# Kernel tuning notes

Measured on AMD Instinct MI355X. Metric: run time of the kernel, lower is better.

The kernel has to match this reference:

```python
import jax, jax.numpy as jnp
import numpy as np

N_NODES = 50000
N_EDGES = 800000
EMB = 96
HID = 2 * EMB


def setup_inputs() -> dict:
    key = jax.random.key(0)
    ks = jax.random.split(key, 8)
    h = jax.random.normal(ks[0], (N_NODES, EMB), dtype=jnp.float32)
    edge_attr = jax.random.normal(ks[1], (N_EDGES, EMB), dtype=jnp.float32)
    src = jax.random.randint(ks[2], (N_EDGES,), 0, N_NODES, dtype=jnp.int32)
    dst = jax.random.randint(ks[3], (N_EDGES,), 0, N_NODES, dtype=jnp.int32)
    W1 = jax.random.normal(ks[4], (EMB, HID), dtype=jnp.float32) * (1.0 / np.sqrt(EMB))
    b1 = jnp.zeros((HID,), dtype=jnp.float32)
    W2 = jax.random.normal(ks[5], (HID, EMB), dtype=jnp.float32) * (1.0 / np.sqrt(HID))
    b2 = jnp.zeros((EMB,), dtype=jnp.float32)
    eps = jnp.zeros((1,), dtype=jnp.float32)
    return {"h": h, "edge_attr": edge_attr, "src": src, "dst": dst,
            "W1": W1, "b1": b1, "W2": W2, "b2": b2, "eps": eps}


def reference(h, edge_attr, src, dst, W1, b1, W2, b2, eps):
    # message: m_e = h[src_e] + edge_attr_e   -> [E, EMB]
    m = h[src] + edge_attr
    # reduce: sum messages per destination node -> [N, EMB]
    aggr = jax.ops.segment_sum(m, dst, num_segments=N_NODES)
    # 2-layer MLP: Linear(EMB, 2*EMB) -> ReLU -> Linear(2*EMB, EMB)
    hidden = jax.nn.relu(aggr @ W1 + b1)
    mlp_out = hidden @ W2 + b2
    # GIN update: (1 + eps) * h + MLP(aggr)
    out = (1.0 + eps[0]) * h + mlp_out
    return out
```

## Files before the change

### kernel.cpp

```cpp
#include <hip/hip_runtime.h>

#define N_NODES 50000
#define N_EDGES 800000
#define EMB 96
#define HID 192

typedef __attribute__((ext_vector_type(8))) short short8;
typedef __attribute__((ext_vector_type(4))) float f32x4;
typedef __attribute__((ext_vector_type(4))) unsigned short ushort4v;

static __device__ __forceinline__ unsigned short f2bf(float f) {
    union { float f; unsigned int u; } v; v.f = f;
    unsigned int u = v.u;
    return (unsigned short)((u + 0x7FFFu + ((u >> 16) & 1u)) >> 16);
}

__global__ __launch_bounds__(256) void hist_kernel(
    const int* __restrict__ dst, int* __restrict__ counts)
{
    int e = blockIdx.x * 256 + threadIdx.x;
    if (e < N_EDGES) atomicAdd(&counts[dst[e]], 1);
}

__global__ __launch_bounds__(1024) void scan_kernel(
    const int* __restrict__ counts, int* __restrict__ offsets)
{
    __shared__ int wave_sums[16];
    int t = threadIdx.x;
    int lane = t & 63, wave = t >> 6;
    int running = 0;
    for (int base = 0; base < N_NODES; base += 1024) {
        int v = (base + t < N_NODES) ? counts[base + t] : 0;
        int x = v;
        #pragma unroll
        for (int d = 1; d < 64; d <<= 1) {
            int y = __shfl_up(x, d);
            if (lane >= d) x += y;
        }
        if (lane == 63) wave_sums[wave] = x;
        __syncthreads();
        if (t < 16) {
            int s = wave_sums[t];
            #pragma unroll
            for (int d = 1; d < 16; d <<= 1) {
                int y = __shfl_up(s, d);
                if (t >= d) s += y;
            }
            wave_sums[t] = s;
        }
        __syncthreads();
        int woff = wave ? wave_sums[wave - 1] : 0;
        if (base + t < N_NODES) offsets[base + t] = running + woff + x - v;
        int total = wave_sums[15];
        __syncthreads();
        running += total;
    }
    if (t == 0) offsets[N_NODES] = running;
}

__global__ __launch_bounds__(256) void fill_kernel(
    const int* __restrict__ src, const int* __restrict__ dst,
    const int* __restrict__ offsets, int* __restrict__ cursor,
    int2* __restrict__ pairs)
{
    int e = blockIdx.x * 256 + threadIdx.x;
    if (e < N_EDGES) {
        int d = dst[e];
        int pos = offsets[d] + atomicAdd(&cursor[d], 1);
        pairs[pos] = make_int2(e, src[e]);
    }
}

__global__ __launch_bounds__(256) void conv_kernel(
    const float* __restrict__ W1, const float* __restrict__ W2,
    unsigned short* __restrict__ W1t, unsigned short* __restrict__ W2t)
{
    int i = blockIdx.x * 256 + threadIdx.x;
    if (i < EMB * HID) {
        int n = i / EMB, k = i % EMB;
        W1t[i] = f2bf(W1[(size_t)k * HID + n]);
    } else if (i < 2 * EMB * HID) {
        int j = i - EMB * HID;
        int n = j / HID, k = j % HID;
        W2t[j] = f2bf(W2[(size_t)k * EMB + n]);
    }
}

__global__ __launch_bounds__(192) void gather_kernel(
    const float4* __restrict__ h4, const float4* __restrict__ ea4,
    const int* __restrict__ offsets, const int2* __restrict__ pairs,
    unsigned short* __restrict__ aggr_bf)
{
    int n = blockIdx.x * 8 + threadIdx.x / 24;
    int c = threadIdx.x % 24;
    if (n >= N_NODES) return;
    int beg = offsets[n], end = offsets[n + 1];
    float4 acc = make_float4(0.f, 0.f, 0.f, 0.f);
    int i = beg;
    int2 p = (i < end) ? pairs[i] : make_int2(0, 0);
    while (i < end) {
        int2 cur = p;
        ++i;
        if (i < end) p = pairs[i];
        float4 a = ea4[(size_t)cur.x * 24 + c];
        float4 b = h4[(size_t)cur.y * 24 + c];
        acc.x += a.x + b.x;
        acc.y += a.y + b.y;
        acc.z += a.z + b.z;
        acc.w += a.w + b.w;
    }
    ushort4v o;
    o.x = f2bf(acc.x); o.y = f2bf(acc.y); o.z = f2bf(acc.z); o.w = f2bf(acc.w);
    *(ushort4v*)(aggr_bf + (size_t)n * EMB + c * 4) = o;
}

__global__ __launch_bounds__(256) void mlp1_mfma(
    const unsigned short* __restrict__ aggr_bf,
    const unsigned short* __restrict__ W1t,
    const float* __restrict__ b1,
    unsigned short* __restrict__ hidden_bf)
{
    __shared__ unsigned short sW[HID * 104];
    int t = threadIdx.x;
    const unsigned int* srcp = (const unsigned int*)W1t;
    for (int i = t; i < HID * (EMB / 2); i += 256) {
        int n = i / (EMB / 2), c = i % (EMB / 2);
        *(unsigned int*)&sW[n * 104 + c * 2] = srcp[(size_t)n * (EMB / 2) + c];
    }
    __syncthreads();
    int wave = t >> 6, lane = t & 63;
    int m0 = (blockIdx.x * 4 + wave) * 16;
    if (m0 >= N_NODES) return;
    int quad = lane >> 4, col = lane & 15;
    f32x4 acc[12];
    #pragma unroll
    for (int c = 0; c < 12; ++c) acc[c] = (f32x4){0.f, 0.f, 0.f, 0.f};
    int m = m0 + col;
    #pragma unroll
    for (int ks = 0; ks < 3; ++ks) {
        short8 af = *(const short8*)(aggr_bf + (size_t)m * EMB + ks * 32 + quad * 8);
        #pragma unroll
        for (int c = 0; c < 12; ++c) {
            short8 bf = *(const short8*)(sW + (c * 16 + col) * 104 + ks * 32 + quad * 8);
            acc[c] = __builtin_amdgcn_mfma_f32_16x16x32_bf16(af, bf, acc[c], 0, 0, 0);
        }
    }
    #pragma unroll
    for (int c = 0; c < 12; ++c) {
        float bias = b1[c * 16 + col];
        #pragma unroll
        for (int r = 0; r < 4; ++r) {
            int row = m0 + quad * 4 + r;
            float v = fmaxf(acc[c][r] + bias, 0.f);
            hidden_bf[(size_t)row * HID + c * 16 + col] = f2bf(v);
        }
    }
}

__global__ __launch_bounds__(256) void mlp2_mfma(
    const unsigned short* __restrict__ hidden_bf,
    const unsigned short* __restrict__ W2t,
    const float* __restrict__ b2,
    const float* __restrict__ h,
    const float* __restrict__ eps,
    float* __restrict__ out)
{
    __shared__ unsigned short sW[EMB * 200];
    int t = threadIdx.x;
    const unsigned int* srcp = (const unsigned int*)W2t;
    for (int i = t; i < EMB * (HID / 2); i += 256) {
        int n = i / (HID / 2), c = i % (HID / 2);
        *(unsigned int*)&sW[n * 200 + c * 2] = srcp[(size_t)n * (HID / 2) + c];
    }
    __syncthreads();
    int wave = t >> 6, lane = t & 63;
    int m0 = (blockIdx.x * 4 + wave) * 16;
    if (m0 >= N_NODES) return;
    int quad = lane >> 4, col = lane & 15;
    f32x4 acc[6];
    #pragma unroll
    for (int c = 0; c < 6; ++c) acc[c] = (f32x4){0.f, 0.f, 0.f, 0.f};
    int m = m0 + col;
    #pragma unroll
    for (int ks = 0; ks < 6; ++ks) {
        short8 af = *(const short8*)(hidden_bf + (size_t)m * HID + ks * 32 + quad * 8);
        #pragma unroll
        for (int c = 0; c < 6; ++c) {
            short8 bf = *(const short8*)(sW + (c * 16 + col) * 200 + ks * 32 + quad * 8);
            acc[c] = __builtin_amdgcn_mfma_f32_16x16x32_bf16(af, bf, acc[c], 0, 0, 0);
        }
    }
    float s = 1.f + eps[0];
    #pragma unroll
    for (int c = 0; c < 6; ++c) {
        float bias = b2[c * 16 + col];
        #pragma unroll
        for (int r = 0; r < 4; ++r) {
            int row = m0 + quad * 4 + r;
            size_t idx = (size_t)row * EMB + c * 16 + col;
            out[idx] = acc[c][r] + bias + s * h[idx];
        }
    }
}

extern "C" void kernel_launch(void* const* d_in, const int* in_sizes, int n_in,
                              void* d_out, int out_size, void* d_ws, size_t ws_size,
                              hipStream_t stream) {
    const float* h         = (const float*)d_in[0];
    const float* edge_attr = (const float*)d_in[1];
    const int*   src       = (const int*)d_in[2];
    const int*   dst       = (const int*)d_in[3];
    const float* W1        = (const float*)d_in[4];
    const float* b1        = (const float*)d_in[5];
    const float* W2        = (const float*)d_in[6];
    const float* b2        = (const float*)d_in[7];
    const float* eps       = (const float*)d_in[8];
    float* out = (float*)d_out;

    unsigned char* wsp = (unsigned char*)d_ws;
    unsigned short* aggr_bf   = (unsigned short*)wsp; wsp += (size_t)N_NODES * EMB * 2;
    unsigned short* hidden_bf = (unsigned short*)wsp; wsp += (size_t)N_NODES * HID * 2;
    unsigned short* W1t       = (unsigned short*)wsp; wsp += (size_t)EMB * HID * 2;
    unsigned short* W2t       = (unsigned short*)wsp; wsp += (size_t)EMB * HID * 2;
    int2* pairs   = (int2*)wsp; wsp += (size_t)N_EDGES * sizeof(int2);
    int*  offsets = (int*)wsp;  wsp += (size_t)(N_NODES + 1) * sizeof(int);
    int*  counts  = (int*)wsp;  wsp += (size_t)N_NODES * sizeof(int);
    int*  cursor  = (int*)wsp;

    hipMemsetAsync(counts, 0, (size_t)2 * N_NODES * sizeof(int), stream);

    hist_kernel<<<(N_EDGES + 255) / 256, 256, 0, stream>>>(dst, counts);
    scan_kernel<<<1, 1024, 0, stream>>>(counts, offsets);
    fill_kernel<<<(N_EDGES + 255) / 256, 256, 0, stream>>>(src, dst, offsets, cursor, pairs);
    conv_kernel<<<(2 * EMB * HID + 255) / 256, 256, 0, stream>>>(W1, W2, W1t, W2t);
    gather_kernel<<<(N_NODES + 7) / 8, 192, 0, stream>>>(
        (const float4*)h, (const float4*)edge_attr, offsets, pairs, aggr_bf);

    mlp1_mfma<<<(N_NODES / 16 + 3) / 4, 256, 0, stream>>>(aggr_bf, W1t, b1, hidden_bf);
    mlp2_mfma<<<(N_NODES / 16 + 3) / 4, 256, 0, stream>>>(hidden_bf, W2t, b2, h, eps, out);
}
```

Baseline: 613.1 us.

## Fuse MLP layers, merge hist/conv kernels, unroll gather, prefetch scan loads

```diff
diff --git a/kernel.cpp b/kernel.cpp
--- a/kernel.cpp
+++ b/kernel.cpp
@@ -5,6 +5,9 @@
 #define EMB 96
 #define HID 192
 
+#define HIST_BLOCKS ((N_EDGES + 255) / 256)
+#define CONV_BLOCKS ((2 * EMB * HID + 255) / 256)
+
 typedef __attribute__((ext_vector_type(8))) short short8;
 typedef __attribute__((ext_vector_type(4))) float f32x4;
 typedef __attribute__((ext_vector_type(4))) unsigned short ushort4v;
@@ -15,11 +18,26 @@
     return (unsigned short)((u + 0x7FFFu + ((u >> 16) & 1u)) >> 16);
 }
 
-__global__ __launch_bounds__(256) void hist_kernel(
-    const int* __restrict__ dst, int* __restrict__ counts)
-{
-    int e = blockIdx.x * 256 + threadIdx.x;
-    if (e < N_EDGES) atomicAdd(&counts[dst[e]], 1);
+__global__ __launch_bounds__(256) void hist_conv_kernel(
+    const int* __restrict__ dst, int* __restrict__ counts,
+    const float* __restrict__ W1, const float* __restrict__ W2,
+    unsigned short* __restrict__ W1t, unsigned short* __restrict__ W2t)
+{
+    int b = blockIdx.x;
+    if (b < HIST_BLOCKS) {
+        int e = b * 256 + threadIdx.x;
+        if (e < N_EDGES) atomicAdd(&counts[dst[e]], 1);
+    } else {
+        int i = (b - HIST_BLOCKS) * 256 + threadIdx.x;
+        if (i < EMB * HID) {
+            int n = i / EMB, k = i % EMB;
+            W1t[i] = f2bf(W1[(size_t)k * HID + n]);
+        } else if (i < 2 * EMB * HID) {
+            int j = i - EMB * HID;
+            int n = j / HID, k = j % HID;
+            W2t[j] = f2bf(W2[(size_t)k * EMB + n]);
+        }
+    }
 }
 
 __global__ __launch_bounds__(1024) void scan_kernel(
@@ -29,8 +47,11 @@
     int t = threadIdx.x;
     int lane = t & 63, wave = t >> 6;
     int running = 0;
+    int v_next = (t < N_NODES) ? counts[t] : 0;
     for (int base = 0; base < N_NODES; base += 1024) {
-        int v = (base + t < N_NODES) ? counts[base + t] : 0;
+        int v = v_next;
+        int nidx = base + 1024 + t;
+        v_next = (nidx < N_NODES) ? counts[nidx] : 0;
         int x = v;
         #pragma unroll
         for (int d = 1; d < 64; d <<= 1) {
@@ -71,23 +92,8 @@
     }
 }
 
-__global__ __launch_bounds__(256) void conv_kernel(
-    const float* __restrict__ W1, const float* __restrict__ W2,
-    unsigned short* __restrict__ W1t, unsigned short* __restrict__ W2t)
-{
-    int i = blockIdx.x * 256 + threadIdx.x;
-    if (i < EMB * HID) {
-        int n = i / EMB, k = i % EMB;
-        W1t[i] = f2bf(W1[(size_t)k * HID + n]);
-    } else if (i < 2 * EMB * HID) {
-        int j = i - EMB * HID;
-        int n = j / HID, k = j % HID;
-        W2t[j] = f2bf(W2[(size_t)k * EMB + n]);
-    }
-}
-
-__global__ __launch_bounds__(192) void gather_kernel(
-    const float4* __restrict__ h4, const float4* __restrict__ ea4,
+__global__ __launch_bounds__(192) void gather_kernel4(
+    const f32x4* __restrict__ h4, const f32x4* __restrict__ ea4,
     const int* __restrict__ offsets, const int2* __restrict__ pairs,
     unsigned short* __restrict__ aggr_bf)
 {
@@ -95,110 +101,106 @@
     int c = threadIdx.x % 24;
     if (n >= N_NODES) return;
     int beg = offsets[n], end = offsets[n + 1];
-    float4 acc = make_float4(0.f, 0.f, 0.f, 0.f);
+    f32x4 a0 = {0.f, 0.f, 0.f, 0.f}, a1 = a0, a2 = a0, a3 = a0;
     int i = beg;
-    int2 p = (i < end) ? pairs[i] : make_int2(0, 0);
-    while (i < end) {
-        int2 cur = p;
-        ++i;
-        if (i < end) p = pairs[i];
-        float4 a = ea4[(size_t)cur.x * 24 + c];
-        float4 b = h4[(size_t)cur.y * 24 + c];
-        acc.x += a.x + b.x;
-        acc.y += a.y + b.y;
-        acc.z += a.z + b.z;
-        acc.w += a.w + b.w;
-    }
+    for (; i + 4 <= end; i += 4) {
+        int2 q0 = pairs[i], q1 = pairs[i + 1], q2 = pairs[i + 2], q3 = pairs[i + 3];
+        f32x4 e0 = __builtin_nontemporal_load(&ea4[(size_t)q0.x * 24 + c]);
+        f32x4 e1 = __builtin_nontemporal_load(&ea4[(size_t)q1.x * 24 + c]);
+        f32x4 e2 = __builtin_nontemporal_load(&ea4[(size_t)q2.x * 24 + c]);
+        f32x4 e3 = __builtin_nontemporal_load(&ea4[(size_t)q3.x * 24 + c]);
+        f32x4 g0 = h4[(size_t)q0.y * 24 + c];
+        f32x4 g1 = h4[(size_t)q1.y * 24 + c];
+        f32x4 g2 = h4[(size_t)q2.y * 24 + c];
+        f32x4 g3 = h4[(size_t)q3.y * 24 + c];
+        a0 += e0 + g0;
+        a1 += e1 + g1;
+        a2 += e2 + g2;
+        a3 += e3 + g3;
+    }
+    for (; i < end; ++i) {
+        int2 q = pairs[i];
+        f32x4 e = __builtin_nontemporal_load(&ea4[(size_t)q.x * 24 + c]);
+        f32x4 g = h4[(size_t)q.y * 24 + c];
+        a0 += e + g;
+    }
+    f32x4 acc = (a0 + a1) + (a2 + a3);
     ushort4v o;
     o.x = f2bf(acc.x); o.y = f2bf(acc.y); o.z = f2bf(acc.z); o.w = f2bf(acc.w);
     *(ushort4v*)(aggr_bf + (size_t)n * EMB + c * 4) = o;
 }
 
-__global__ __launch_bounds__(256) void mlp1_mfma(
+__global__ __launch_bounds__(256) void mlp_fused(
     const unsigned short* __restrict__ aggr_bf,
-    const unsigned short* __restrict__ W1t,
-    const float* __restrict__ b1,
-    unsigned short* __restrict__ hidden_bf)
-{
-    __shared__ unsigned short sW[HID * 104];
+    const unsigned short* __restrict__ W1t, const float* __restrict__ b1,
+    const unsigned short* __restrict__ W2t, const float* __restrict__ b2,
+    const float* __restrict__ h, const float* __restrict__ eps,
+    float* __restrict__ out)
+{
+    __shared__ unsigned short sW1[HID * 104];
     int t = threadIdx.x;
-    const unsigned int* srcp = (const unsigned int*)W1t;
+    const unsigned int* p1 = (const unsigned int*)W1t;
     for (int i = t; i < HID * (EMB / 2); i += 256) {
-        int n = i / (EMB / 2), c = i % (EMB / 2);
-        *(unsigned int*)&sW[n * 104 + c * 2] = srcp[(size_t)n * (EMB / 2) + c];
+        int n = i / (EMB / 2), c2 = i % (EMB / 2);
+        *(unsigned int*)&sW1[n * 104 + c2 * 2] = p1[(size_t)n * (EMB / 2) + c2];
     }
     __syncthreads();
+
     int wave = t >> 6, lane = t & 63;
     int m0 = (blockIdx.x * 4 + wave) * 16;
-    if (m0 >= N_NODES) return;
+    bool active = (m0 < N_NODES);
     int quad = lane >> 4, col = lane & 15;
-    f32x4 acc[12];
+    int m = m0 + col;
+
+    f32x4 acc1[12];
     #pragma unroll
-    for (int c = 0; c < 12; ++c) acc[c] = (f32x4){0.f, 0.f, 0.f, 0.f};
-    int m = m0 + col;
-    #pragma unroll
-    for (int ks = 0; ks < 3; ++ks) {
-        short8 af = *(const short8*)(aggr_bf + (size_t)m * EMB + ks * 32 + quad * 8);
+    for (int c = 0; c < 12; ++c) acc1[c] = (f32x4){0.f, 0.f, 0.f, 0.f};
+    if (active) {
+        #pragma unroll
+        for (int ks = 0; ks < 3; ++ks) {
+            short8 af = *(const short8*)(aggr_bf + (size_t)m * EMB + ks * 32 + quad * 8);
+            #pragma unroll
+            for (int c = 0; c < 12; ++c) {
+                short8 bf = *(const short8*)(sW1 + (c * 16 + col) * 104 + ks * 32 + quad * 8);
+                acc1[c] = __builtin_amdgcn_mfma_f32_16x16x32_bf16(af, bf, acc1[c], 0, 0, 0);
+            }
+        }
+    }
+    __syncthreads();
+
+    if (active) {
+        unsigned short* sH = sW1 + wave * (16 * 200);
         #pragma unroll
         for (int c = 0; c < 12; ++c) {
-            short8 bf = *(const short8*)(sW + (c * 16 + col) * 104 + ks * 32 + quad * 8);
-            acc[c] = __builtin_amdgcn_mfma_f32_16x16x32_bf16(af, bf, acc[c], 0, 0, 0);
-        }
-    }
-    #pragma unroll
-    for (int c = 0; c < 12; ++c) {
-        float bias = b1[c * 16 + col];
-        #pragma unroll
-        for (int r = 0; r < 4; ++r) {
-            int row = m0 + quad * 4 + r;
-            float v = fmaxf(acc[c][r] + bias, 0.f);
-            hidden_bf[(size_t)row * HID + c * 16 + col] = f2bf(v);
-        }
-    }
-}
-
-__global__ __launch_bounds__(256) void mlp2_mfma(
-    const unsigned short* __restrict__ hidden_bf,
-    const unsigned short* __restrict__ W2t,
-    const float* __restrict__ b2,
-    const float* __restrict__ h,
-    const float* __restrict__ eps,
-    float* __restrict__ out)
-{
-    __shared__ unsigned short sW[EMB * 200];
-    int t = threadIdx.x;
-    const unsigned int* srcp = (const unsigned int*)W2t;
-    for (int i = t; i < EMB * (HID / 2); i += 256) {
-        int n = i / (HID / 2), c = i % (HID / 2);
-        *(unsigned int*)&sW[n * 200 + c * 2] = srcp[(size_t)n * (HID / 2) + c];
-    }
-    __syncthreads();
-    int wave = t >> 6, lane = t & 63;
-    int m0 = (blockIdx.x * 4 + wave) * 16;
-    if (m0 >= N_NODES) return;
-    int quad = lane >> 4, col = lane & 15;
-    f32x4 acc[6];
-    #pragma unroll
-    for (int c = 0; c < 6; ++c) acc[c] = (f32x4){0.f, 0.f, 0.f, 0.f};
-    int m = m0 + col;
-    #pragma unroll
-    for (int ks = 0; ks < 6; ++ks) {
-        short8 af = *(const short8*)(hidden_bf + (size_t)m * HID + ks * 32 + quad * 8);
+            float bias = b1[c * 16 + col];
+            #pragma unroll
+            for (int r = 0; r < 4; ++r) {
+                int lr = quad * 4 + r;
+                sH[lr * 200 + c * 16 + col] = f2bf(fmaxf(acc1[c][r] + bias, 0.f));
+            }
+        }
+        f32x4 acc2[6];
+        #pragma unroll
+        for (int c = 0; c < 6; ++c) acc2[c] = (f32x4){0.f, 0.f, 0.f, 0.f};
+        #pragma unroll
+        for (int ks = 0; ks < 6; ++ks) {
+            short8 af = *(const short8*)(sH + col * 200 + ks * 32 + quad * 8);
+            #pragma unroll
+            for (int c = 0; c < 6; ++c) {
+                short8 bf = *(const short8*)(W2t + (size_t)(c * 16 + col) * HID + ks * 32 + quad * 8);
+                acc2[c] = __builtin_amdgcn_mfma_f32_16x16x32_bf16(af, bf, acc2[c], 0, 0, 0);
+            }
+        }
+        float s = 1.f + eps[0];
         #pragma unroll
         for (int c = 0; c < 6; ++c) {
-            short8 bf = *(const short8*)(sW + (c * 16 + col) * 200 + ks * 32 + quad * 8);
-            acc[c] = __builtin_amdgcn_mfma_f32_16x16x32_bf16(af, bf, acc[c], 0, 0, 0);
-        }
-    }
-    float s = 1.f + eps[0];
-    #pragma unroll
-    for (int c = 0; c < 6; ++c) {
-        float bias = b2[c * 16 + col];
-        #pragma unroll
-        for (int r = 0; r < 4; ++r) {
-            int row = m0 + quad * 4 + r;
-            size_t idx = (size_t)row * EMB + c * 16 + col;
-            out[idx] = acc[c][r] + bias + s * h[idx];
+            float bias = b2[c * 16 + col];
+            #pragma unroll
+            for (int r = 0; r < 4; ++r) {
+                int row = m0 + quad * 4 + r;
+                size_t idx = (size_t)row * EMB + c * 16 + col;
+                out[idx] = acc2[c][r] + bias + s * h[idx];
+            }
         }
     }
 }
@@ -218,10 +220,9 @@
     float* out = (float*)d_out;
 
     unsigned char* wsp = (unsigned char*)d_ws;
-    unsigned short* aggr_bf   = (unsigned short*)wsp; wsp += (size_t)N_NODES * EMB * 2;
-    unsigned short* hidden_bf = (unsigned short*)wsp; wsp += (size_t)N_NODES * HID * 2;
-    unsigned short* W1t       = (unsigned short*)wsp; wsp += (size_t)EMB * HID * 2;
-    unsigned short* W2t       = (unsigned short*)wsp; wsp += (size_t)EMB * HID * 2;
+    unsigned short* aggr_bf = (unsigned short*)wsp; wsp += (size_t)N_NODES * EMB * 2;
+    unsigned short* W1t     = (unsigned short*)wsp; wsp += (size_t)EMB * HID * 2;
+    unsigned short* W2t     = (unsigned short*)wsp; wsp += (size_t)EMB * HID * 2;
     int2* pairs   = (int2*)wsp; wsp += (size_t)N_EDGES * sizeof(int2);
     int*  offsets = (int*)wsp;  wsp += (size_t)(N_NODES + 1) * sizeof(int);
     int*  counts  = (int*)wsp;  wsp += (size_t)N_NODES * sizeof(int);
@@ -229,13 +230,12 @@
 
     hipMemsetAsync(counts, 0, (size_t)2 * N_NODES * sizeof(int), stream);
 
-    hist_kernel<<<(N_EDGES + 255) / 256, 256, 0, stream>>>(dst, counts);
+    hist_conv_kernel<<<HIST_BLOCKS + CONV_BLOCKS, 256, 0, stream>>>(
+        dst, counts, W1, W2, W1t, W2t);
     scan_kernel<<<1, 1024, 0, stream>>>(counts, offsets);
     fill_kernel<<<(N_EDGES + 255) / 256, 256, 0, stream>>>(src, dst, offsets, cursor, pairs);
-    conv_kernel<<<(2 * EMB * HID + 255) / 256, 256, 0, stream>>>(W1, W2, W1t, W2t);
-    gather_kernel<<<(N_NODES + 7) / 8, 192, 0, stream>>>(
-        (const float4*)h, (const float4*)edge_attr, offsets, pairs, aggr_bf);
-
-    mlp1_mfma<<<(N_NODES / 16 + 3) / 4, 256, 0, stream>>>(aggr_bf, W1t, b1, hidden_bf);
-    mlp2_mfma<<<(N_NODES / 16 + 3) / 4, 256, 0, stream>>>(hidden_bf, W2t, b2, h, eps, out);
-}
+    gather_kernel4<<<(N_NODES + 7) / 8, 192, 0, stream>>>(
+        (const f32x4*)h, (const f32x4*)edge_attr, offsets, pairs, aggr_bf);
+    mlp_fused<<<(N_NODES / 16 + 3) / 4, 256, 0, stream>>>(
+        aggr_bf, W1t, b1, W2t, b2, h, eps, out);
+}
```

Result: faster. 596.7 us (-2.7%).
